# Kernel optimization log

Measured on AMD Instinct MI355X. Metric: run time of the kernel, lower is better.

Reference implementation:

```python
import jax, jax.numpy as jnp
import numpy as np

D_MODEL = 512
N_HEADS = 8
HEAD_DIM = D_MODEL // N_HEADS
B, L, S = 4, 2048, 2048


def setup_inputs() -> dict:
    key = jax.random.key(0)
    ks = jax.random.split(key, 16)
    std = 1.0 / np.sqrt(D_MODEL)
    inp = {
        'queries': jax.random.normal(ks[0], (B, L, D_MODEL), jnp.float32),
        'keys': jax.random.normal(ks[1], (B, S, D_MODEL), jnp.float32),
        'values': jax.random.normal(ks[2], (B, S, D_MODEL), jnp.float32),
        'tau': jax.random.uniform(ks[3], (B,), jnp.float32, 0.5, 1.5),
        'delta': jax.random.normal(ks[4], (B,), jnp.float32) * 0.1,
        'Wq': jax.random.normal(ks[5], (D_MODEL, D_MODEL), jnp.float32) * std,
        'bq': jnp.zeros((D_MODEL,), jnp.float32),
        'Wk': jax.random.normal(ks[6], (D_MODEL, D_MODEL), jnp.float32) * std,
        'bk': jnp.zeros((D_MODEL,), jnp.float32),
        'Wv': jax.random.normal(ks[7], (D_MODEL, D_MODEL), jnp.float32) * std,
        'bv': jnp.zeros((D_MODEL,), jnp.float32),
        'Wo': jax.random.normal(ks[8], (D_MODEL, D_MODEL), jnp.float32) * std,
        'bo': jnp.zeros((D_MODEL,), jnp.float32),
    }
    return inp


def reference(queries, keys, values, tau, delta, Wq, bq, Wk, bk, Wv, bv, Wo, bo):
    Bq, Lq, _ = queries.shape
    Sk = keys.shape[1]
    H, E = N_HEADS, HEAD_DIM
    # projections -> [B, L, H, E]
    q = (queries @ Wq + bq).reshape(Bq, Lq, H, E)
    k = (keys @ Wk + bk).reshape(Bq, Sk, H, E)
    v = (values @ Wv + bv).reshape(Bq, Sk, H, E)
    scale = 1.0 / jnp.sqrt(jnp.float32(E))
    # scores: [B, H, L, S]
    scores = jnp.einsum('blhe,bshe->bhls', q, k)
    scores = scores * tau[:, None, None, None] + delta[:, None, None, None]
    A = jax.nn.softmax(scale * scores, axis=-1)  # dropout is identity in eval
    out = jnp.einsum('bhls,bshd->blhd', A, v).reshape(Bq, Lq, H * E)
    return out @ Wo + bo
```

## Files before the change

kernel.cpp:

```cpp
#include <hip/hip_runtime.h>
#include <stdint.h>

#define NB 4
#define LQ 2048
#define DM 512
#define NH 8
#define EH 64
#define MT (NB*LQ)
#define QBLK 128

typedef __attribute__((ext_vector_type(4)))  float f32x4;
typedef __attribute__((ext_vector_type(8)))  __bf16 bf16x8;
typedef __attribute__((ext_vector_type(8)))  unsigned short u16x8;
typedef __attribute__((ext_vector_type(4)))  float float4_t;

static __device__ __forceinline__ unsigned short f2bf(float f) {
  unsigned int u = __builtin_bit_cast(unsigned int, f);
  u += 0x7fffu + ((u >> 16) & 1u);
  return (unsigned short)(u >> 16);
}

static __device__ __forceinline__ void gload16(const void* g, void* l) {
  __builtin_amdgcn_global_load_lds(
      (__attribute__((address_space(1))) unsigned int*)(g),
      (__attribute__((address_space(3))) unsigned int*)(l), 16, 0, 0);
}

static __device__ __forceinline__ unsigned int cvt_pk_bf16(float lo, float hi) {
  unsigned int r;
  asm("v_cvt_pk_bf16_f32 %0, %1, %2" : "=v"(r) : "v"(lo), "v"(hi));
  return r;
}

extern "C" __global__ __launch_bounds__(256) void k_cast_x(
    const float* __restrict__ q, const float* __restrict__ k,
    const float* __restrict__ v, unsigned short* __restrict__ x) {
  int z = blockIdx.y;
  const float* src = (z == 0) ? q : ((z == 1) ? k : v);
  unsigned short* dst = x + (size_t)z * MT * DM;
  size_t i = ((size_t)blockIdx.x * 256 + threadIdx.x) * 8;
  float4_t a = *(const float4_t*)(src + i);
  float4_t b = *(const float4_t*)(src + i + 4);
  u16x8 r;
  r[0]=f2bf(a[0]); r[1]=f2bf(a[1]); r[2]=f2bf(a[2]); r[3]=f2bf(a[3]);
  r[4]=f2bf(b[0]); r[5]=f2bf(b[1]); r[6]=f2bf(b[2]); r[7]=f2bf(b[3]);
  *(u16x8*)(dst + i) = r;
}

extern "C" __global__ __launch_bounds__(256) void k_cast_wt(
    const float* __restrict__ wq, const float* __restrict__ wk,
    const float* __restrict__ wv, const float* __restrict__ wo,
    unsigned short* __restrict__ wt) {
  __shared__ float tile[64][65];
  int z = blockIdx.z;
  const float* w = (z==0)?wq : (z==1)?wk : (z==2)?wv : wo;
  unsigned short* dst = wt + (size_t)z * DM * DM;
  int kb = blockIdx.y * 64, nb = blockIdx.x * 64;
  int t = threadIdx.x;
  int r = t >> 2, c0 = (t & 3) * 16;
  #pragma unroll
  for (int i = 0; i < 16; i += 4) {
    float4_t v4 = *(const float4_t*)(w + (size_t)(kb + r) * DM + nb + c0 + i);
    tile[r][c0+i]   = v4[0]; tile[r][c0+i+1] = v4[1];
    tile[r][c0+i+2] = v4[2]; tile[r][c0+i+3] = v4[3];
  }
  __syncthreads();
  u16x8 o0, o1;
  #pragma unroll
  for (int i = 0; i < 8; ++i) o0[i] = f2bf(tile[c0+i][r]);
  #pragma unroll
  for (int i = 0; i < 8; ++i) o1[i] = f2bf(tile[c0+8+i][r]);
  *(u16x8*)(dst + (size_t)(nb + r) * DM + kb + c0)     = o0;
  *(u16x8*)(dst + (size_t)(nb + r) * DM + kb + c0 + 8) = o1;
}

extern "C" __global__ __launch_bounds__(256) void k_gemm_qkv(
    const unsigned short* __restrict__ X, const unsigned short* __restrict__ WT,
    const float* __restrict__ bq, const float* __restrict__ bk,
    const float* __restrict__ bv, unsigned short* __restrict__ out) {
  int z = blockIdx.z;
  const unsigned short* A  = X  + (size_t)z * MT * DM;
  const unsigned short* Bt = WT + (size_t)z * DM * DM;
  const float* bias = (z==0)?bq : (z==1)?bk : bv;
  unsigned short* dst = out + (size_t)z * MT * DM;

  __shared__ unsigned short As[2][128][32];
  __shared__ unsigned short Bs[2][128][32];

  int m0 = blockIdx.y * 128;
  int n0 = blockIdx.x * 128;
  int t = threadIdx.x;
  int lane = t & 63;
  int w = t >> 6;
  int wr = w >> 1, wc = w & 1;
  int g = lane >> 4, r15 = lane & 15;

  f32x4 acc[4][4];
  #pragma unroll
  for (int i=0;i<4;i++)
    #pragma unroll
    for (int j=0;j<4;j++)
      #pragma unroll
      for (int e=0;e<4;e++) acc[i][j][e] = 0.f;

  auto stage = [&](int bb, int kt) {
    int k0 = kt * 32;
    int sblk = (t & 3) ^ ((t >> 3) & 3);
    #pragma unroll
    for (int j=0;j<2;j++) {
      int o = t*16 + j*4096;
      int row = o >> 6;
      gload16(A  + (size_t)(m0+row)*DM + k0 + sblk*8, (char*)(&As[bb][0][0]) + o);
      gload16(Bt + (size_t)(n0+row)*DM + k0 + sblk*8, (char*)(&Bs[bb][0][0]) + o);
    }
  };

  stage(0, 0);
  __syncthreads();
  int buf = 0;
  for (int kt = 0; kt < DM/32; ++kt) {
    if (kt + 1 < DM/32) stage(buf ^ 1, kt + 1);
    bf16x8 af[4], bfr[4];
    #pragma unroll
    for (int mi=0;mi<4;mi++) {
      int row = wr*64 + mi*16 + r15;
      int blk = g ^ ((row >> 1) & 3);
      af[mi] = *(const bf16x8*)(&As[buf][row][blk*8]);
    }
    #pragma unroll
    for (int ni=0;ni<4;ni++) {
      int row = wc*64 + ni*16 + r15;
      int blk = g ^ ((row >> 1) & 3);
      bfr[ni] = *(const bf16x8*)(&Bs[buf][row][blk*8]);
    }
    #pragma unroll
    for (int mi=0;mi<4;mi++)
      #pragma unroll
      for (int ni=0;ni<4;ni++)
        acc[mi][ni] = __builtin_amdgcn_mfma_f32_16x16x32_bf16(af[mi], bfr[ni], acc[mi][ni], 0, 0, 0);
    __syncthreads();
    buf ^= 1;
  }
  #pragma unroll
  for (int ni=0;ni<4;ni++) {
    int n = n0 + wc*64 + ni*16 + r15;
    float bia = bias[n];
    int h = n >> 6, e = n & 63;
    #pragma unroll
    for (int mi=0;mi<4;mi++) {
      #pragma unroll
      for (int rg=0;rg<4;rg++) {
        int m = m0 + wr*64 + mi*16 + g*4 + rg;
        int b = m >> 11, s = m & 2047;
        dst[((size_t)((b*NH + h)*LQ + s))*EH + e] = f2bf(acc[mi][ni][rg] + bia);
      }
    }
  }
}

extern "C" __global__ __launch_bounds__(256) void k_flash(
    const unsigned short* __restrict__ qkv, const float* __restrict__ tau,
    unsigned short* __restrict__ aout) {
  int bid = blockIdx.x;
  int orig = (bid & 7) * 64 + (bid >> 3);
  int qblk = orig & 15;
  int bh = orig >> 4;
  int batch = bh >> 3, h = bh & 7;
  const unsigned short* Qh = qkv + (size_t)bh * LQ * EH + (size_t)qblk * QBLK * EH;
  const unsigned short* Kh = qkv + (size_t)MT * DM     + (size_t)bh * LQ * EH;
  const unsigned short* Vh = qkv + (size_t)2 * MT * DM + (size_t)bh * LQ * EH;

  __shared__ unsigned short Qs[QBLK][64];
  __shared__ unsigned short Ks[2][64][64];
  __shared__ unsigned short Vt[2][64][64];

  int t = threadIdx.x;
  int lane = t & 63;
  int wv = t >> 6;
  int q4 = lane & 15;
  int g  = lane >> 4;
  float C2 = tau[batch] * 0.18033688011112042f;

  #pragma unroll
  for (int j=0;j<4;j++) {
    int o = t*16 + j*4096;
    int row = o >> 7;
    int sblk = (t & 7) ^ ((row ^ (row>>3)) & 7);
    gload16(Qh + (size_t)row*EH + sblk*8, (char*)(&Qs[0][0]) + o);
  }

  auto stageK = [&](int bb, int kt) {
    #pragma unroll
    for (int j=0;j<2;j++) {
      int o = t*16 + j*4096;
      int row = o >> 7;
      int sblk = (t & 7) ^ ((row ^ (row>>3)) & 7);
      gload16(Kh + (size_t)(kt*64 + row)*EH + sblk*8, (char*)(&Ks[bb][0][0]) + o);
    }
  };
  u16x8 vr0, vr1;
  auto loadV = [&](int kt) {
    int kv = (t >> 3) * 2, e0 = (t & 7) * 8;
    const unsigned short* vp = Vh + (size_t)(kt*64 + kv)*EH + e0;
    vr0 = *(const u16x8*)vp;
    vr1 = *(const u16x8*)(vp + EH);
  };
  auto writeVT = [&](int bb) {
    int kv = (t >> 3) * 2, e0 = (t & 7) * 8;
    #pragma unroll
    for (int i=0;i<8;i++) {
      int e = e0 + i;
      int kvs = kv ^ (((e ^ (e>>3)) & 7) << 3);
      *(unsigned int*)(&Vt[bb][e][kvs]) = (unsigned int)vr0[i] | ((unsigned int)vr1[i] << 16);
    }
  };

  stageK(0, 0);
  loadV(0);
  writeVT(0);
  __syncthreads();

  bf16x8 qf[2][2];
  #pragma unroll
  for (int qt=0;qt<2;qt++) {
    int row = wv*32 + qt*16 + q4;
    int S = (row ^ (row>>3)) & 7;
    #pragma unroll
    for (int st=0;st<2;st++) {
      int blk = (st*4 + g) ^ S;
      qf[qt][st] = *(const bf16x8*)(&Qs[row][blk*8]);
    }
  }
  asm volatile("s_waitcnt lgkmcnt(0)" ::: "memory");
  __builtin_amdgcn_sched_barrier(0);

  unsigned short (*Pw)[64] = (unsigned short (*)[64])(&Qs[wv*32][0]);

  const f32x4 Z4 = {0.f, 0.f, 0.f, 0.f};
  f32x4 oacc[4][2];
  #pragma unroll
  for (int a=0;a<4;a++)
    #pragma unroll
    for (int b2=0;b2<2;b2++)
      #pragma unroll
      for (int e=0;e<4;e++) oacc[a][b2][e] = 0.f;
  float lsp[2] = {0.f, 0.f};

  int buf = 0;
  for (int kt = 0; kt < 32; ++kt) {
    if (kt + 1 < 32) { stageK(buf^1, kt+1); loadV(kt+1); }

    f32x4 sac[4][2];
    __builtin_amdgcn_s_setprio(1);
    #pragma unroll
    for (int kvt=0; kvt<4; ++kvt) {
      int row = kvt*16 + q4;
      int blk = g ^ ((row ^ (row>>3)) & 7);
      bf16x8 kf = *(const bf16x8*)(&Ks[buf][row][blk*8]);
      sac[kvt][0] = __builtin_amdgcn_mfma_f32_16x16x32_bf16(kf, qf[0][0], Z4, 0,0,0);
      sac[kvt][1] = __builtin_amdgcn_mfma_f32_16x16x32_bf16(kf, qf[1][0], Z4, 0,0,0);
    }
    #pragma unroll
    for (int kvt=0; kvt<4; ++kvt) {
      int row = kvt*16 + q4;
      int blk = (4 + g) ^ ((row ^ (row>>3)) & 7);
      bf16x8 kf = *(const bf16x8*)(&Ks[buf][row][blk*8]);
      sac[kvt][0] = __builtin_amdgcn_mfma_f32_16x16x32_bf16(kf, qf[0][1], sac[kvt][0], 0,0,0);
      sac[kvt][1] = __builtin_amdgcn_mfma_f32_16x16x32_bf16(kf, qf[1][1], sac[kvt][1], 0,0,0);
    }
    __builtin_amdgcn_s_setprio(0);

    #pragma unroll
    for (int qt=0; qt<2; ++qt) {
      int qrow = qt*16 + q4;
      int sw = ((qrow ^ (qrow>>3)) & 7) << 3;
      #pragma unroll
      for (int kvt=0; kvt<4; ++kvt) {
        float p0 = __builtin_amdgcn_exp2f(sac[kvt][qt][0] * C2);
        float p1 = __builtin_amdgcn_exp2f(sac[kvt][qt][1] * C2);
        float p2 = __builtin_amdgcn_exp2f(sac[kvt][qt][2] * C2);
        float p3 = __builtin_amdgcn_exp2f(sac[kvt][qt][3] * C2);
        lsp[qt] += (p0 + p1) + (p2 + p3);
        int kv0 = (kvt*16 + g*4) ^ sw;
        *(unsigned int*)(&Pw[qrow][kv0])     = cvt_pk_bf16(p0, p1);
        *(unsigned int*)(&Pw[qrow][kv0 + 2]) = cvt_pk_bf16(p2, p3);
      }
    }
    asm volatile("s_waitcnt lgkmcnt(0)" ::: "memory");
    __builtin_amdgcn_sched_barrier(0);

    #pragma unroll
    for (int kvst=0; kvst<2; ++kvst) {
      bf16x8 pf[2];
      #pragma unroll
      for (int qt=0; qt<2; ++qt) {
        int qrow = qt*16 + q4;
        int blk = (kvst*4 + g) ^ ((qrow ^ (qrow>>3)) & 7);
        pf[qt] = *(const bf16x8*)(&Pw[qrow][blk*8]);
      }
      __builtin_amdgcn_s_setprio(1);
      #pragma unroll
      for (int et=0; et<4; ++et) {
        int row = et*16 + q4;
        int blk = (kvst*4 + g) ^ ((row ^ (row>>3)) & 7);
        bf16x8 vf = *(const bf16x8*)(&Vt[buf][row][blk*8]);
        #pragma unroll
        for (int qt=0; qt<2; ++qt)
          oacc[et][qt] = __builtin_amdgcn_mfma_f32_16x16x32_bf16(vf, pf[qt], oacc[et][qt], 0,0,0);
      }
      __builtin_amdgcn_s_setprio(0);
    }

    if (kt + 1 < 32) writeVT(buf^1);
    __syncthreads();
    buf ^= 1;
  }

  #pragma unroll
  for (int qt=0; qt<2; ++qt) {
    float s = lsp[qt];
    s += __shfl_xor(s, 16, 64);
    s += __shfl_xor(s, 32, 64);
    float inv = 1.f / s;
    int q = qblk*QBLK + wv*32 + qt*16 + q4;
    unsigned short* rowp = aout + (size_t)(batch*LQ + q)*DM + h*EH;
    #pragma unroll
    for (int et=0; et<4; ++et) {
      #pragma unroll
      for (int rg=0; rg<4; rg+=2) {
        int e = et*16 + g*4 + rg;
        *(unsigned int*)(rowp + e) = cvt_pk_bf16(oacc[et][qt][rg] * inv, oacc[et][qt][rg+1] * inv);
      }
    }
  }
}

extern "C" __global__ __launch_bounds__(256) void k_gemm_out(
    const unsigned short* __restrict__ A, const unsigned short* __restrict__ WT,
    const float* __restrict__ bo, float* __restrict__ out) {
  const unsigned short* Bt = WT + (size_t)3 * DM * DM;

  __shared__ unsigned short As[2][128][32];
  __shared__ unsigned short Bs[2][128][32];

  int m0 = blockIdx.y * 128;
  int n0 = blockIdx.x * 128;
  int t = threadIdx.x;
  int lane = t & 63;
  int w = t >> 6;
  int wr = w >> 1, wc = w & 1;
  int g = lane >> 4, r15 = lane & 15;

  f32x4 acc[4][4];
  #pragma unroll
  for (int i=0;i<4;i++)
    #pragma unroll
    for (int j=0;j<4;j++)
      #pragma unroll
      for (int e=0;e<4;e++) acc[i][j][e] = 0.f;

  auto stage = [&](int bb, int kt) {
    int k0 = kt * 32;
    int sblk = (t & 3) ^ ((t >> 3) & 3);
    #pragma unroll
    for (int j=0;j<2;j++) {
      int o = t*16 + j*4096;
      int row = o >> 6;
      gload16(A  + (size_t)(m0+row)*DM + k0 + sblk*8, (char*)(&As[bb][0][0]) + o);
      gload16(Bt + (size_t)(n0+row)*DM + k0 + sblk*8, (char*)(&Bs[bb][0][0]) + o);
    }
  };

  stage(0, 0);
  __syncthreads();
  int buf = 0;
  for (int kt = 0; kt < DM/32; ++kt) {
    if (kt + 1 < DM/32) stage(buf ^ 1, kt + 1);
    bf16x8 af[4], bfr[4];
    #pragma unroll
    for (int mi=0;mi<4;mi++) {
      int row = wr*64 + mi*16 + r15;
      int blk = g ^ ((row >> 1) & 3);
      af[mi] = *(const bf16x8*)(&As[buf][row][blk*8]);
    }
    #pragma unroll
    for (int ni=0;ni<4;ni++) {
      int row = wc*64 + ni*16 + r15;
      int blk = g ^ ((row >> 1) & 3);
      bfr[ni] = *(const bf16x8*)(&Bs[buf][row][blk*8]);
    }
    #pragma unroll
    for (int mi=0;mi<4;mi++)
      #pragma unroll
      for (int ni=0;ni<4;ni++)
        acc[mi][ni] = __builtin_amdgcn_mfma_f32_16x16x32_bf16(af[mi], bfr[ni], acc[mi][ni], 0, 0, 0);
    __syncthreads();
    buf ^= 1;
  }
  #pragma unroll
  for (int ni=0;ni<4;ni++) {
    int n = n0 + wc*64 + ni*16 + r15;
    float bia = bo[n];
    #pragma unroll
    for (int mi=0;mi<4;mi++) {
      #pragma unroll
      for (int rg=0;rg<4;rg++) {
        int m = m0 + wr*64 + mi*16 + g*4 + rg;
        out[(size_t)m*DM + n] = acc[mi][ni][rg] + bia;
      }
    }
  }
}

extern "C" void kernel_launch(void* const* d_in, const int* in_sizes, int n_in,
                              void* d_out, int out_size, void* d_ws, size_t ws_size,
                              hipStream_t stream) {
  const float* queries = (const float*)d_in[0];
  const float* keys    = (const float*)d_in[1];
  const float* values  = (const float*)d_in[2];
  const float* tau     = (const float*)d_in[3];
  const float* Wq = (const float*)d_in[5];
  const float* bq = (const float*)d_in[6];
  const float* Wk = (const float*)d_in[7];
  const float* bk = (const float*)d_in[8];
  const float* Wv = (const float*)d_in[9];
  const float* bv = (const float*)d_in[10];
  const float* Wo = (const float*)d_in[11];
  const float* bo = (const float*)d_in[12];
  float* out = (float*)d_out;

  char* ws = (char*)d_ws;
  unsigned short* WT   = (unsigned short*)(ws);
  unsigned short* X    = (unsigned short*)(ws + (2u  << 20));
  unsigned short* QKV  = (unsigned short*)(ws + (26u << 20));
  unsigned short* AOut = (unsigned short*)(ws + (50u << 20));

  k_cast_x  <<<dim3(2048, 3), dim3(256), 0, stream>>>(queries, keys, values, X);
  k_cast_wt <<<dim3(8, 8, 4), dim3(256), 0, stream>>>(Wq, Wk, Wv, Wo, WT);
  k_gemm_qkv<<<dim3(4, 64, 3), dim3(256), 0, stream>>>(X, WT, bq, bk, bv, QKV);
  k_flash   <<<dim3(512), dim3(256), 0, stream>>>(QKV, tau, AOut);
  k_gemm_out<<<dim3(4, 64), dim3(256), 0, stream>>>(AOut, WT, bo, out);
}
```

Before: 112.0 us.

## Pre-transpose V globally and load K/V fragments directly into registers

Adds a separate kernel that transposes V into a [bh][E][S] layout in workspace, reusing the X buffer region. The flash kernel drops its LDS staging of Q, K and V and loads MFMA fragments straight from global memory into registers. It double-buffers K fragments across an unrolled pair of iterations and removes the per-tile __syncthreads. This removes LDS traffic and block-wide syncs, but adds a kernel launch plus an extra global round trip for V, and relies on L2/cache hits for repeated K/V reads across the 16 query blocks. It also sets launch_bounds(256,2).

```diff
diff --git a/kernel.cpp b/kernel.cpp
--- a/kernel.cpp
+++ b/kernel.cpp
@@ -158,9 +158,32 @@
   }
 }
 
-extern "C" __global__ __launch_bounds__(256) void k_flash(
-    const unsigned short* __restrict__ qkv, const float* __restrict__ tau,
-    unsigned short* __restrict__ aout) {
+extern "C" __global__ __launch_bounds__(256) void k_vt(
+    const unsigned short* __restrict__ qkv, unsigned short* __restrict__ vtg) {
+  __shared__ unsigned short tile[64][65];
+  int bh = blockIdx.y;
+  int s0 = blockIdx.x * 64;
+  const unsigned short* Vh = qkv + (size_t)2*MT*DM + (size_t)bh*LQ*EH;
+  unsigned short* Ot = vtg + (size_t)bh*EH*LQ;
+  int t = threadIdx.x;
+  int r = t >> 2, c0 = (t & 3) * 16;
+  u16x8 a = *(const u16x8*)(Vh + (size_t)(s0 + r)*EH + c0);
+  u16x8 b = *(const u16x8*)(Vh + (size_t)(s0 + r)*EH + c0 + 8);
+  #pragma unroll
+  for (int i=0;i<8;i++) { tile[r][c0+i] = a[i]; tile[r][c0+8+i] = b[i]; }
+  __syncthreads();
+  u16x8 o0, o1;
+  #pragma unroll
+  for (int i=0;i<8;i++) o0[i] = tile[c0+i][r];
+  #pragma unroll
+  for (int i=0;i<8;i++) o1[i] = tile[c0+8+i][r];
+  *(u16x8*)(Ot + (size_t)r*LQ + s0 + c0)     = o0;
+  *(u16x8*)(Ot + (size_t)r*LQ + s0 + c0 + 8) = o1;
+}
+
+extern "C" __global__ __launch_bounds__(256, 2) void k_flash(
+    const unsigned short* __restrict__ qkv, const unsigned short* __restrict__ vtg,
+    const float* __restrict__ tau, unsigned short* __restrict__ aout) {
   int bid = blockIdx.x;
   int orig = (bid & 7) * 64 + (bid >> 3);
   int qblk = orig & 15;
@@ -168,11 +191,9 @@
   int batch = bh >> 3, h = bh & 7;
   const unsigned short* Qh = qkv + (size_t)bh * LQ * EH + (size_t)qblk * QBLK * EH;
   const unsigned short* Kh = qkv + (size_t)MT * DM     + (size_t)bh * LQ * EH;
-  const unsigned short* Vh = qkv + (size_t)2 * MT * DM + (size_t)bh * LQ * EH;
-
-  __shared__ unsigned short Qs[QBLK][64];
-  __shared__ unsigned short Ks[2][64][64];
-  __shared__ unsigned short Vt[2][64][64];
+  const unsigned short* VT = vtg + (size_t)bh * EH * LQ;
+
+  __shared__ unsigned short Pall[4][32][64];
 
   int t = threadIdx.x;
   int lane = t & 63;
@@ -181,60 +202,14 @@
   int g  = lane >> 4;
   float C2 = tau[batch] * 0.18033688011112042f;
 
-  #pragma unroll
-  for (int j=0;j<4;j++) {
-    int o = t*16 + j*4096;
-    int row = o >> 7;
-    int sblk = (t & 7) ^ ((row ^ (row>>3)) & 7);
-    gload16(Qh + (size_t)row*EH + sblk*8, (char*)(&Qs[0][0]) + o);
-  }
-
-  auto stageK = [&](int bb, int kt) {
-    #pragma unroll
-    for (int j=0;j<2;j++) {
-      int o = t*16 + j*4096;
-      int row = o >> 7;
-      int sblk = (t & 7) ^ ((row ^ (row>>3)) & 7);
-      gload16(Kh + (size_t)(kt*64 + row)*EH + sblk*8, (char*)(&Ks[bb][0][0]) + o);
-    }
-  };
-  u16x8 vr0, vr1;
-  auto loadV = [&](int kt) {
-    int kv = (t >> 3) * 2, e0 = (t & 7) * 8;
-    const unsigned short* vp = Vh + (size_t)(kt*64 + kv)*EH + e0;
-    vr0 = *(const u16x8*)vp;
-    vr1 = *(const u16x8*)(vp + EH);
-  };
-  auto writeVT = [&](int bb) {
-    int kv = (t >> 3) * 2, e0 = (t & 7) * 8;
-    #pragma unroll
-    for (int i=0;i<8;i++) {
-      int e = e0 + i;
-      int kvs = kv ^ (((e ^ (e>>3)) & 7) << 3);
-      *(unsigned int*)(&Vt[bb][e][kvs]) = (unsigned int)vr0[i] | ((unsigned int)vr1[i] << 16);
-    }
-  };
-
-  stageK(0, 0);
-  loadV(0);
-  writeVT(0);
-  __syncthreads();
+  unsigned short (*Pw)[64] = Pall[wv];
 
   bf16x8 qf[2][2];
   #pragma unroll
-  for (int qt=0;qt<2;qt++) {
-    int row = wv*32 + qt*16 + q4;
-    int S = (row ^ (row>>3)) & 7;
-    #pragma unroll
-    for (int st=0;st<2;st++) {
-      int blk = (st*4 + g) ^ S;
-      qf[qt][st] = *(const bf16x8*)(&Qs[row][blk*8]);
-    }
-  }
-  asm volatile("s_waitcnt lgkmcnt(0)" ::: "memory");
-  __builtin_amdgcn_sched_barrier(0);
-
-  unsigned short (*Pw)[64] = (unsigned short (*)[64])(&Qs[wv*32][0]);
+  for (int qt=0;qt<2;qt++)
+    #pragma unroll
+    for (int st=0;st<2;st++)
+      qf[qt][st] = *(const bf16x8*)(Qh + (size_t)(wv*32 + qt*16 + q4)*EH + st*32 + g*8);
 
   const f32x4 Z4 = {0.f, 0.f, 0.f, 0.f};
   f32x4 oacc[4][2];
@@ -246,27 +221,34 @@
       for (int e=0;e<4;e++) oacc[a][b2][e] = 0.f;
   float lsp[2] = {0.f, 0.f};
 
-  int buf = 0;
-  for (int kt = 0; kt < 32; ++kt) {
-    if (kt + 1 < 32) { stageK(buf^1, kt+1); loadV(kt+1); }
+  auto loadK = [&](bf16x8 (&kf)[4][2], int kt) {
+    #pragma unroll
+    for (int kvt=0;kvt<4;kvt++)
+      #pragma unroll
+      for (int st=0;st<2;st++)
+        kf[kvt][st] = *(const bf16x8*)(Kh + (size_t)(kt*64 + kvt*16 + q4)*EH + st*32 + g*8);
+  };
+
+  auto step = [&](int kt, bf16x8 (&kc)[4][2], bf16x8 (&kn)[4][2], bool pre) {
+    bf16x8 vc[4][2];
+    #pragma unroll
+    for (int et=0;et<4;et++)
+      #pragma unroll
+      for (int kvst=0;kvst<2;kvst++)
+        vc[et][kvst] = *(const bf16x8*)(VT + (size_t)(et*16 + q4)*LQ + kt*64 + kvst*32 + g*8);
+    if (pre) loadK(kn, kt + 1);
 
     f32x4 sac[4][2];
     __builtin_amdgcn_s_setprio(1);
     #pragma unroll
     for (int kvt=0; kvt<4; ++kvt) {
-      int row = kvt*16 + q4;
-      int blk = g ^ ((row ^ (row>>3)) & 7);
-      bf16x8 kf = *(const bf16x8*)(&Ks[buf][row][blk*8]);
-      sac[kvt][0] = __builtin_amdgcn_mfma_f32_16x16x32_bf16(kf, qf[0][0], Z4, 0,0,0);
-      sac[kvt][1] = __builtin_amdgcn_mfma_f32_16x16x32_bf16(kf, qf[1][0], Z4, 0,0,0);
+      sac[kvt][0] = __builtin_amdgcn_mfma_f32_16x16x32_bf16(kc[kvt][0], qf[0][0], Z4, 0,0,0);
+      sac[kvt][1] = __builtin_amdgcn_mfma_f32_16x16x32_bf16(kc[kvt][0], qf[1][0], Z4, 0,0,0);
     }
     #pragma unroll
     for (int kvt=0; kvt<4; ++kvt) {
-      int row = kvt*16 + q4;
-      int blk = (4 + g) ^ ((row ^ (row>>3)) & 7);
-      bf16x8 kf = *(const bf16x8*)(&Ks[buf][row][blk*8]);
-      sac[kvt][0] = __builtin_amdgcn_mfma_f32_16x16x32_bf16(kf, qf[0][1], sac[kvt][0], 0,0,0);
-      sac[kvt][1] = __builtin_amdgcn_mfma_f32_16x16x32_bf16(kf, qf[1][1], sac[kvt][1], 0,0,0);
+      sac[kvt][0] = __builtin_amdgcn_mfma_f32_16x16x32_bf16(kc[kvt][1], qf[0][1], sac[kvt][0], 0,0,0);
+      sac[kvt][1] = __builtin_amdgcn_mfma_f32_16x16x32_bf16(kc[kvt][1], qf[1][1], sac[kvt][1], 0,0,0);
     }
     __builtin_amdgcn_s_setprio(0);
 
@@ -301,19 +283,18 @@
       __builtin_amdgcn_s_setprio(1);
       #pragma unroll
       for (int et=0; et<4; ++et) {
-        int row = et*16 + q4;
-        int blk = (kvst*4 + g) ^ ((row ^ (row>>3)) & 7);
-        bf16x8 vf = *(const bf16x8*)(&Vt[buf][row][blk*8]);
-        #pragma unroll
-        for (int qt=0; qt<2; ++qt)
-          oacc[et][qt] = __builtin_amdgcn_mfma_f32_16x16x32_bf16(vf, pf[qt], oacc[et][qt], 0,0,0);
+        oacc[et][0] = __builtin_amdgcn_mfma_f32_16x16x32_bf16(vc[et][kvst], pf[0], oacc[et][0], 0,0,0);
+        oacc[et][1] = __builtin_amdgcn_mfma_f32_16x16x32_bf16(vc[et][kvst], pf[1], oacc[et][1], 0,0,0);
       }
       __builtin_amdgcn_s_setprio(0);
     }
-
-    if (kt + 1 < 32) writeVT(buf^1);
-    __syncthreads();
-    buf ^= 1;
+  };
+
+  bf16x8 kA[4][2], kB[4][2];
+  loadK(kA, 0);
+  for (int kt = 0; kt < 32; kt += 2) {
+    step(kt,     kA, kB, true);
+    step(kt + 1, kB, kA, kt + 2 < 32);
   }
 
   #pragma unroll
@@ -432,12 +413,14 @@
   char* ws = (char*)d_ws;
   unsigned short* WT   = (unsigned short*)(ws);
   unsigned short* X    = (unsigned short*)(ws + (2u  << 20));
+  unsigned short* VTg  = (unsigned short*)(ws + (2u  << 20));
   unsigned short* QKV  = (unsigned short*)(ws + (26u << 20));
   unsigned short* AOut = (unsigned short*)(ws + (50u << 20));
 
   k_cast_x  <<<dim3(2048, 3), dim3(256), 0, stream>>>(queries, keys, values, X);
   k_cast_wt <<<dim3(8, 8, 4), dim3(256), 0, stream>>>(Wq, Wk, Wv, Wo, WT);
   k_gemm_qkv<<<dim3(4, 64, 3), dim3(256), 0, stream>>>(X, WT, bq, bk, bv, QKV);
-  k_flash   <<<dim3(512), dim3(256), 0, stream>>>(QKV, tau, AOut);
+  k_vt      <<<dim3(32, 32), dim3(256), 0, stream>>>(QKV, VTg);
+  k_flash   <<<dim3(512), dim3(256), 0, stream>>>(QKV, VTg, tau, AOut);
   k_gemm_out<<<dim3(4, 64), dim3(256), 0, stream>>>(AOut, WT, bo, out);
 }
```

New measurement: 177.7 us. 58.7% more time.
